# Performance work log

Measured on AMD Instinct MI355X. Metric: run time of the kernel, lower is better.

## Reference

```python
import jax, jax.numpy as jnp
import numpy as np

B, S, D = 2, 2048, 2048
H, KVH, HD = 8, 1, 256          # query heads, kv heads, head_dim (GQA: n_rep = H // KVH)
ROPE_THETA = 10000.0
NEG_INF = -1e9


def setup_inputs() -> dict:
    key = jax.random.key(0)
    k1, k2, k3, k4, k5 = jax.random.split(key, 5)
    hidden_states = jax.random.normal(k1, (B, S, D), dtype=jnp.float32)
    # additive causal mask: 0 where allowed, -inf where masked, shape (B,1,S,S)
    causal = jnp.tril(jnp.ones((S, S), dtype=bool))
    attention_mask = jnp.where(causal, 0.0, NEG_INF).astype(jnp.float32)
    attention_mask = jnp.broadcast_to(attention_mask[None, None], (B, 1, S, S))
    position_ids = jnp.broadcast_to(jnp.arange(S, dtype=jnp.int32)[None, :], (B, S))
    sc = 0.02
    Wq = jax.random.normal(k2, (H * HD, D), dtype=jnp.float32) * sc   # torch Linear weight layout [out,in]
    Wk = jax.random.normal(k3, (KVH * HD, D), dtype=jnp.float32) * sc
    Wv = jax.random.normal(k4, (KVH * HD, D), dtype=jnp.float32) * sc
    Wo = jax.random.normal(k5, (D, H * HD), dtype=jnp.float32) * sc
    return {"hidden_states": hidden_states, "attention_mask": attention_mask,
            "position_ids": position_ids, "Wq": Wq, "Wk": Wk, "Wv": Wv, "Wo": Wo}


def _rotate_half(x):
    x1, x2 = jnp.split(x, 2, axis=-1)
    return jnp.concatenate((-x2, x1), axis=-1)


def _rope_cos_sin(position_ids):
    inv_freq = 1.0 / (ROPE_THETA ** (jnp.arange(0, HD, 2, dtype=jnp.float32) / HD))  # [HD/2]
    freqs = position_ids.astype(jnp.float32)[:, :, None] * inv_freq[None, None, :]   # [B,S,HD/2]
    emb = jnp.concatenate((freqs, freqs), axis=-1)                                   # [B,S,HD]
    return jnp.cos(emb)[:, None], jnp.sin(emb)[:, None]                              # [B,1,S,HD]


def reference(hidden_states, attention_mask, position_ids, Wq, Wk, Wv, Wo):
    q = (hidden_states @ Wq.T).reshape(B, S, H, HD).transpose(0, 2, 1, 3)     # [B,H,S,HD]
    k = (hidden_states @ Wk.T).reshape(B, S, KVH, HD).transpose(0, 2, 1, 3)   # [B,KVH,S,HD]
    v = (hidden_states @ Wv.T).reshape(B, S, KVH, HD).transpose(0, 2, 1, 3)
    cos, sin = _rope_cos_sin(position_ids)
    q = q * cos + _rotate_half(q) * sin
    k = k * cos + _rotate_half(k) * sin
    n_rep = H // KVH
    k = jnp.repeat(k, n_rep, axis=1)                                          # repeat_kv -> [B,H,S,HD]
    v = jnp.repeat(v, n_rep, axis=1)
    scores = jnp.einsum('bhqd,bhkd->bhqk', q, k) / jnp.sqrt(jnp.float32(HD))
    scores = scores + attention_mask
    attn = jax.nn.softmax(scores, axis=-1)                                    # dropout p=0 (eval)
    ctx = jnp.einsum('bhqk,bhkd->bhqd', attn, v)
    ctx = ctx.transpose(0, 2, 1, 3).reshape(B, S, H * HD)
    out = ctx @ Wo.T
    return out, attn
```

## Files before the change

kernel.cpp:

```cpp
#include <hip/hip_runtime.h>
#include <hip/hip_bf16.h>
#include <math.h>

typedef __bf16 bf16_t;
typedef __bf16 bf16x8 __attribute__((ext_vector_type(8)));
typedef float  f32x4  __attribute__((ext_vector_type(4)));

#define DEV __device__ __forceinline__

constexpr int B_   = 2;
constexpr int S_   = 2048;
constexpr int D_   = 2048;
constexpr int H_   = 8;
constexpr int HD_  = 256;
constexpr int NQKV_ = H_ * HD_ + 2 * HD_;
constexpr int TOK_ = B_ * S_;
constexpr int CHK_ = 64 * HD_;

#if defined(__has_builtin)
#if __has_builtin(__builtin_amdgcn_global_load_lds)
#define HAS_GLLDS 1
#endif
#endif

DEV void stage16(const bf16_t* g, bf16_t* l) {
#ifdef HAS_GLLDS
  __builtin_amdgcn_global_load_lds((const __attribute__((address_space(1))) void*)g,
                                   (__attribute__((address_space(3))) void*)l, 16, 0, 0);
#else
  *(bf16x8*)l = *(const bf16x8*)g;
#endif
}

__global__ void cast_inputs(const float* __restrict__ hs, const float* __restrict__ wq,
                            const float* __restrict__ wk, const float* __restrict__ wv,
                            const float* __restrict__ wo,
                            bf16_t* __restrict__ Xb, bf16_t* __restrict__ Wqkvb,
                            bf16_t* __restrict__ Wob) {
  const size_t i = (size_t)blockIdx.x * blockDim.x + threadIdx.x;
  const size_t NHS = (size_t)TOK_ * D_;
  const size_t NWQ = (size_t)H_ * HD_ * D_;
  const size_t NWK = (size_t)HD_ * D_;
  if (i < NHS) Xb[i] = (bf16_t)hs[i];
  if (i < NWQ) { Wqkvb[i] = (bf16_t)wq[i]; Wob[i] = (bf16_t)wo[i]; }
  if (i < NWK) { Wqkvb[NWQ + i] = (bf16_t)wk[i]; Wqkvb[NWQ + NWK + i] = (bf16_t)wv[i]; }
}

template <bool CBF16>
__global__ __launch_bounds__(256, 2)
void gemm_bt(const bf16_t* __restrict__ Ab, const bf16_t* __restrict__ Bg,
             void* __restrict__ Cv, int K, int lda, int ldb, int ldc)
{
  const int bn = blockIdx.x, bm = blockIdx.y;
  const int m0 = bm * 128, n0 = bn * 128;

  __shared__ __align__(16) bf16_t Asm[128 * 32];
  __shared__ __align__(16) bf16_t Bsm[128 * 32];

  const int tid  = threadIdx.x;
  const int l    = tid & 63;
  const int w    = tid >> 6;
  const int wm   = (w >> 1) * 64;
  const int wn   = (w & 1) * 64;
  const int lrow = l & 15;
  const int quad = l >> 4;

  f32x4 acc[4][4] = {};

  for (int k0 = 0; k0 < K; k0 += 32) {
    __syncthreads();
    #pragma unroll
    for (int c = 0; c < 2; ++c) {
      int chunk = c * 256 + tid;
      int row = chunk >> 2, col = (chunk & 3) << 3;
      stage16(Ab + (size_t)(m0 + row) * lda + (k0 + col), &Asm[row * 32 + col]);
      stage16(Bg + (size_t)(n0 + row) * ldb + (k0 + col), &Bsm[row * 32 + col]);
    }
    __syncthreads();

    bf16x8 af[4], bfr[4];
    #pragma unroll
    for (int i = 0; i < 4; ++i)
      af[i] = *(const bf16x8*)&Asm[(wm + i * 16 + lrow) * 32 + quad * 8];
    #pragma unroll
    for (int j = 0; j < 4; ++j)
      bfr[j] = *(const bf16x8*)&Bsm[(wn + j * 16 + lrow) * 32 + quad * 8];
    #pragma unroll
    for (int i = 0; i < 4; ++i)
      #pragma unroll
      for (int j = 0; j < 4; ++j)
        acc[i][j] = __builtin_amdgcn_mfma_f32_16x16x32_bf16(af[i], bfr[j], acc[i][j], 0, 0, 0);
  }

  #pragma unroll
  for (int i = 0; i < 4; ++i) {
    int row = wm + i * 16 + quad * 4;
    #pragma unroll
    for (int j = 0; j < 4; ++j) {
      int col = n0 + wn + j * 16 + lrow;
      #pragma unroll
      for (int r = 0; r < 4; ++r) {
        if (CBF16) ((bf16_t*)Cv)[(size_t)(m0 + row + r) * ldc + col] = (bf16_t)acc[i][j][r];
        else       ((float*) Cv)[(size_t)(m0 + row + r) * ldc + col] = acc[i][j][r];
      }
    }
  }
}

__global__ void rope_kernel(const bf16_t* __restrict__ qkv, const int* __restrict__ pos_ids,
                            bf16_t* __restrict__ Qh, bf16_t* __restrict__ Kb,
                            bf16_t* __restrict__ K2)
{
  const int t = blockIdx.x;
  const int b = t >> 11, s = t & (S_ - 1);
  const int tid = threadIdx.x;
  const int h = tid >> 5, c = tid & 31;
  const float pos = (float)pos_ids[t];
  const int pdbase = (c & 15) * 8;
  float cs[8], sn[8];
  #pragma unroll
  for (int j = 0; j < 8; ++j) {
    float invf = exp2f((float)(pdbase + j) * -0.103810253f);
    float ang = pos * invf;
    cs[j] = cosf(ang); sn[j] = sinf(ang);
  }
  const float sgn = (c < 16) ? -1.0f : 1.0f;
  const bf16_t* base = qkv + (size_t)t * NQKV_;

  {
    bf16x8 x  = *(const bf16x8*)(base + h * HD_ + c * 8);
    bf16x8 xo = *(const bf16x8*)(base + h * HD_ + (c ^ 16) * 8);
    bf16x8 o;
    #pragma unroll
    for (int j = 0; j < 8; ++j)
      o[j] = (bf16_t)((float)x[j] * cs[j] + sgn * (float)xo[j] * sn[j]);
    *(bf16x8*)(Qh + ((size_t)(b * H_ + h) * S_ + s) * HD_ + c * 8) = o;
  }
  if (h == 0) {
    bf16x8 x  = *(const bf16x8*)(base + D_ + c * 8);
    bf16x8 xo = *(const bf16x8*)(base + D_ + (c ^ 16) * 8);
    bf16x8 o;
    #pragma unroll
    for (int j = 0; j < 8; ++j)
      o[j] = (bf16_t)((float)x[j] * cs[j] + sgn * (float)xo[j] * sn[j]);
    *(bf16x8*)(Kb + (size_t)t * HD_ + c * 8) = o;
    const int chunk = s >> 6, key = s & 63;
    *(bf16x8*)(K2 + (size_t)(b * 32 + chunk) * CHK_ + c * 512 + key * 8) = o;
  }
}

__global__ void v_trans(const bf16_t* __restrict__ qkv, bf16_t* __restrict__ V2)
{
  const int blk = blockIdx.x;
  const int s0 = (blk & 31) * 64;
  const int b = blk >> 5;
  const int tid = threadIdx.x;
  __shared__ bf16_t L[64][264];
  #pragma unroll
  for (int it = 0; it < 8; ++it) {
    int gi = it * 256 + tid;
    int r = gi >> 5, cc = gi & 31;
    *(bf16x8*)&L[r][cc * 8] =
        *(const bf16x8*)(qkv + ((size_t)b * S_ + s0 + r) * NQKV_ + (D_ + HD_) + cc * 8);
  }
  __syncthreads();
  bf16_t* out = V2 + (size_t)blk * CHK_;
  #pragma unroll
  for (int it = 0; it < 8; ++it) {
    int G = it * 256 + tid;
    bf16x8 o;
    #pragma unroll
    for (int j = 0; j < 8; ++j) o[j] = L[it * 8 + j][tid];
    *(bf16x8*)(out + (size_t)G * 8) = o;
  }
}

constexpr int PSTR = 136;

DEV void compute_S(const bf16_t* __restrict__ K2g, bf16_t* __restrict__ KV,
                   const bf16x8 aq[8], f32x4 accS[8],
                   int kb, int tid, int lrow, int quad)
{
  #pragma unroll
  for (int half = 0; half < 2; ++half) {
    __syncthreads();
    const bf16_t* src = K2g + (size_t)(kb * 2 + half) * CHK_;
    #pragma unroll
    for (int it = 0; it < 8; ++it) {
      int s = it * 256 + tid;
      stage16(src + (size_t)s * 8, KV + s * 8);
    }
    __syncthreads();
    __builtin_amdgcn_s_setprio(1);
    #pragma unroll
    for (int kk = 0; kk < 8; ++kk) {
      bf16x8 bk[4];
      #pragma unroll
      for (int j = 0; j < 4; ++j)
        bk[j] = *(const bf16x8*)&KV[((kk * 4 + quad) * 64 + j * 16 + lrow) * 8];
      #pragma unroll
      for (int j = 0; j < 4; ++j)
        accS[half * 4 + j] =
            __builtin_amdgcn_mfma_f32_16x16x32_bf16(aq[kk], bk[j], accS[half * 4 + j], 0, 0, 0);
    }
    __builtin_amdgcn_s_setprio(0);
  }
}

__global__ __launch_bounds__(256, 2)
void flash_attn(const bf16_t* __restrict__ Qh, const bf16_t* __restrict__ K2,
                const bf16_t* __restrict__ V2, bf16_t* __restrict__ Ctx,
                float* __restrict__ lsum)
{
  const int idx = blockIdx.x;
  int z, qb;
  if (idx < 256) { z = idx & 15; qb = idx >> 4; }
  else           { int j = idx - 256; z = j & 15; qb = 31 - (j >> 4); }
  const int b = z >> 3, h = z & 7;
  const int q0 = qb * 64;
  const bf16_t* Qg  = Qh + ((size_t)z * S_ + q0) * HD_;
  const bf16_t* K2g = K2 + (size_t)b * 32 * CHK_;
  const bf16_t* V2g = V2 + (size_t)b * 32 * CHK_;

  __shared__ __align__(16) bf16_t KV[64 * 256];
  __shared__ __align__(16) bf16_t Pst[4 * 16 * PSTR];

  const int tid = threadIdx.x;
  const int w = tid >> 6, l = tid & 63;
  const int lrow = l & 15, quad = l >> 4;
  const int nkb = (qb >> 1) + 1;
  const float scale = 0.0625f;

  bf16x8 aq[8];
  const bf16_t* qrow = Qg + (size_t)(w * 16 + lrow) * HD_ + quad * 8;
  #pragma unroll
  for (int kk = 0; kk < 8; ++kk) aq[kk] = *(const bf16x8*)(qrow + kk * 32);

  const int rowg0 = q0 + w * 16 + quad * 4;
  float lp[4] = {0.f, 0.f, 0.f, 0.f};
  f32x4 accO[16] = {};
  bf16_t* pw = &Pst[w * 16 * PSTR];

  for (int kb = 0; kb < nkb; ++kb) {
    f32x4 accS[8] = {};
    compute_S(K2g, KV, aq, accS, kb, tid, lrow, quad);

    #pragma unroll
    for (int r = 0; r < 4; ++r) {
      #pragma unroll
      for (int j = 0; j < 8; ++j) {
        int col = kb * 128 + j * 16 + lrow;
        float p = (col <= rowg0 + r) ? __expf(accS[j][r] * scale) : 0.f;
        lp[r] += p;
        pw[(quad * 4 + r) * PSTR + j * 16 + lrow] = (bf16_t)p;
      }
    }
    bf16x8 ap[4];
    #pragma unroll
    for (int kk2 = 0; kk2 < 4; ++kk2)
      ap[kk2] = *(const bf16x8*)&pw[lrow * PSTR + kk2 * 32 + quad * 8];

    #pragma unroll
    for (int half = 0; half < 2; ++half) {
      __syncthreads();
      const bf16_t* src = V2g + (size_t)(kb * 2 + half) * CHK_;
      #pragma unroll
      for (int it = 0; it < 8; ++it) {
        int s = it * 256 + tid;
        stage16(src + (size_t)s * 8, KV + s * 8);
      }
      __syncthreads();
      __builtin_amdgcn_s_setprio(1);
      #pragma unroll
      for (int kkl = 0; kkl < 2; ++kkl) {
        #pragma unroll
        for (int j2 = 0; j2 < 16; ++j2) {
          bf16x8 bv = *(const bf16x8*)&KV[((kkl * 4 + quad) * 256 + j2 * 16 + lrow) * 8];
          accO[j2] = __builtin_amdgcn_mfma_f32_16x16x32_bf16(ap[half * 2 + kkl], bv, accO[j2], 0, 0, 0);
        }
      }
      __builtin_amdgcn_s_setprio(0);
    }
  }

  #pragma unroll
  for (int r = 0; r < 4; ++r) {
    #pragma unroll
    for (int o = 1; o < 16; o <<= 1) lp[r] += __shfl_xor(lp[r], o, 64);
  }
  float inv[4];
  #pragma unroll
  for (int r = 0; r < 4; ++r) inv[r] = 1.0f / lp[r];

  #pragma unroll
  for (int j2 = 0; j2 < 16; ++j2) {
    #pragma unroll
    for (int r = 0; r < 4; ++r) {
      int rowq = q0 + w * 16 + quad * 4 + r;
      Ctx[((size_t)b * S_ + rowq) * D_ + h * HD_ + j2 * 16 + lrow] = (bf16_t)(accO[j2][r] * inv[r]);
    }
  }
  if (lrow == 0) {
    #pragma unroll
    for (int r = 0; r < 4; ++r) lsum[(size_t)z * S_ + rowg0 + r] = lp[r];
  }
}

__global__ __launch_bounds__(256, 2)
void p_writer(const bf16_t* __restrict__ Qh, const bf16_t* __restrict__ Kbp,
              const float* __restrict__ lsum, float* __restrict__ attn)
{
  const int bn = blockIdx.x, bm = blockIdx.y, z = blockIdx.z;
  const int m0 = bm * 128, n0 = bn * 128;
  float* Pg = attn + (size_t)z * S_ * S_;
  const int tid = threadIdx.x;

  if (bn > bm) {
    #pragma unroll
    for (int it = 0; it < 16; ++it) {
      int idx = it * 256 + tid;
      int row = idx >> 5, c4 = idx & 31;
      *(f32x4*)&Pg[(size_t)(m0 + row) * S_ + n0 + c4 * 4] = f32x4{0.f, 0.f, 0.f, 0.f};
    }
    return;
  }

  const bf16_t* Ab = Qh + (size_t)z * S_ * HD_;
  const bf16_t* Bg = Kbp + (size_t)(z >> 3) * S_ * HD_;

  __shared__ __align__(16) bf16_t Asm[128 * 32];
  __shared__ __align__(16) bf16_t Bsm[128 * 32];

  const int l    = tid & 63;
  const int w    = tid >> 6;
  const int wm   = (w >> 1) * 64;
  const int wn   = (w & 1) * 64;
  const int lrow = l & 15;
  const int quad = l >> 4;

  f32x4 acc[4][4] = {};

  for (int k0 = 0; k0 < HD_; k0 += 32) {
    __syncthreads();
    #pragma unroll
    for (int c = 0; c < 2; ++c) {
      int chunk = c * 256 + tid;
      int row = chunk >> 2, col = (chunk & 3) << 3;
      stage16(Ab + (size_t)(m0 + row) * HD_ + (k0 + col), &Asm[row * 32 + col]);
      stage16(Bg + (size_t)(n0 + row) * HD_ + (k0 + col), &Bsm[row * 32 + col]);
    }
    __syncthreads();

    bf16x8 af[4], bfr[4];
    #pragma unroll
    for (int i = 0; i < 4; ++i)
      af[i] = *(const bf16x8*)&Asm[(wm + i * 16 + lrow) * 32 + quad * 8];
    #pragma unroll
    for (int j = 0; j < 4; ++j)
      bfr[j] = *(const bf16x8*)&Bsm[(wn + j * 16 + lrow) * 32 + quad * 8];
    #pragma unroll
    for (int i = 0; i < 4; ++i)
      #pragma unroll
      for (int j = 0; j < 4; ++j)
        acc[i][j] = __builtin_amdgcn_mfma_f32_16x16x32_bf16(af[i], bfr[j], acc[i][j], 0, 0, 0);
  }

  const float scale = 0.0625f;
  #pragma unroll
  for (int i = 0; i < 4; ++i) {
    int row = m0 + wm + i * 16 + quad * 4;
    #pragma unroll
    for (int r = 0; r < 4; ++r) {
      const float il = 1.0f / lsum[(size_t)z * S_ + row + r];
      float* prow = &Pg[(size_t)(row + r) * S_];
      #pragma unroll
      for (int j = 0; j < 4; ++j) {
        int col = n0 + wn + j * 16 + lrow;
        prow[col] = (col <= row + r) ? __expf(acc[i][j][r] * scale) * il : 0.f;
      }
    }
  }
}

extern "C" void kernel_launch(void* const* d_in, const int* in_sizes, int n_in,
                              void* d_out, int out_size, void* d_ws, size_t ws_size,
                              hipStream_t stream)
{
  const float* hs  = (const float*)d_in[0];
  const int*   pos = (const int*)d_in[2];
  const float* wq  = (const float*)d_in[3];
  const float* wk  = (const float*)d_in[4];
  const float* wv  = (const float*)d_in[5];
  const float* wo  = (const float*)d_in[6];

  float* out  = (float*)d_out;
  float* attn = out + (size_t)TOK_ * D_;

  char* ws = (char*)d_ws;
  bf16_t* Xb    = (bf16_t*)(ws);
  bf16_t* Wqkvb = (bf16_t*)(ws + 16777216);
  bf16_t* Wob   = (bf16_t*)(ws + 27262976);
  bf16_t* QKVb  = (bf16_t*)(ws + 35651584);
  bf16_t* Qh    = (bf16_t*)(ws + 56623104);
  bf16_t* Kb    = (bf16_t*)(ws + 73400320);
  bf16_t* V2    = (bf16_t*)(ws + 75497472);
  bf16_t* Ctx   = (bf16_t*)(ws + 77594624);
  float*  lsum  = (float* )(ws + 94371840);
  bf16_t* K2    = (bf16_t*)(ws + 94502912);

  cast_inputs<<<(TOK_ * D_) / 256, 256, 0, stream>>>(hs, wq, wk, wv, wo, Xb, Wqkvb, Wob);
  gemm_bt<true><<<dim3(NQKV_ / 128, TOK_ / 128), 256, 0, stream>>>(
      Xb, Wqkvb, QKVb, D_, D_, D_, NQKV_);
  rope_kernel<<<TOK_, 256, 0, stream>>>(QKVb, pos, Qh, Kb, K2);
  v_trans<<<B_ * 32, 256, 0, stream>>>(QKVb, V2);
  flash_attn<<<512, 256, 0, stream>>>(Qh, K2, V2, Ctx, lsum);
  p_writer<<<dim3(S_ / 128, S_ / 128, B_ * H_), 256, 0, stream>>>(Qh, Kb, lsum, attn);
  gemm_bt<false><<<dim3(D_ / 128, TOK_ / 128), 256, 0, stream>>>(
      Ctx, Wob, out, D_, D_, D_, D_);
}
```

Measured before the change: 622.1 us.

## Use K=64 swizzled LDS tiles, XCD-aware block remap, and overlap V staging with softmax

Moves the shared GEMM mainloop into a helper that stages 64-wide K tiles with an XOR swizzle, halving barrier count and targeting LDS bank conflicts. The gemm and p_writer grids are remapped so consecutive logical tiles land on the same XCD, aiming for better L2 reuse. The attention kernel now issues the first V chunk load before the exp/P-store phase so the global load overlaps softmax work. LDS use per block doubles, which may reduce occupancy, and the remap in p_writer hardcodes the grid size.

```diff
diff --git a/kernel.cpp b/kernel.cpp
--- a/kernel.cpp
+++ b/kernel.cpp
@@ -46,16 +46,55 @@
   if (i < NWK) { Wqkvb[NWQ + i] = (bf16_t)wk[i]; Wqkvb[NWQ + NWK + i] = (bf16_t)wv[i]; }
 }
 
+DEV void tile_k64(const bf16_t* __restrict__ Ab, const bf16_t* __restrict__ Bg,
+                  int K, int lda, int ldb, int m0, int n0,
+                  bf16_t* Asm, bf16_t* Bsm, f32x4 acc[4][4],
+                  int tid, int lrow, int quad, int wm, int wn)
+{
+  const int sw = (lrow & 1) << 2;
+  for (int k0 = 0; k0 < K; k0 += 64) {
+    __syncthreads();
+    #pragma unroll
+    for (int c = 0; c < 4; ++c) {
+      int chunk = c * 256 + tid;
+      int row = chunk >> 3, pg = chunk & 7;
+      int g = pg ^ ((row & 1) << 2);
+      stage16(Ab + (size_t)(m0 + row) * lda + (k0 + g * 8), &Asm[chunk * 8]);
+      stage16(Bg + (size_t)(n0 + row) * ldb + (k0 + g * 8), &Bsm[chunk * 8]);
+    }
+    __syncthreads();
+    #pragma unroll
+    for (int kk = 0; kk < 2; ++kk) {
+      bf16x8 af[4], bfr[4];
+      #pragma unroll
+      for (int i = 0; i < 4; ++i)
+        af[i] = *(const bf16x8*)&Asm[(wm + i * 16 + lrow) * 64 + ((quad + kk * 4) ^ sw) * 8];
+      #pragma unroll
+      for (int j = 0; j < 4; ++j)
+        bfr[j] = *(const bf16x8*)&Bsm[(wn + j * 16 + lrow) * 64 + ((quad + kk * 4) ^ sw) * 8];
+      #pragma unroll
+      for (int i = 0; i < 4; ++i)
+        #pragma unroll
+        for (int j = 0; j < 4; ++j)
+          acc[i][j] = __builtin_amdgcn_mfma_f32_16x16x32_bf16(af[i], bfr[j], acc[i][j], 0, 0, 0);
+    }
+  }
+}
+
 template <bool CBF16>
 __global__ __launch_bounds__(256, 2)
 void gemm_bt(const bf16_t* __restrict__ Ab, const bf16_t* __restrict__ Bg,
              void* __restrict__ Cv, int K, int lda, int ldb, int ldc)
 {
-  const int bn = blockIdx.x, bm = blockIdx.y;
+  const int nwg = gridDim.x * gridDim.y;
+  const int w0  = blockIdx.y * gridDim.x + blockIdx.x;
+  const int q   = nwg >> 3;
+  const int logical = (w0 & 7) * q + (w0 >> 3);
+  const int bm = logical / gridDim.x, bn = logical % gridDim.x;
   const int m0 = bm * 128, n0 = bn * 128;
 
-  __shared__ __align__(16) bf16_t Asm[128 * 32];
-  __shared__ __align__(16) bf16_t Bsm[128 * 32];
+  __shared__ __align__(16) bf16_t Asm[128 * 64];
+  __shared__ __align__(16) bf16_t Bsm[128 * 64];
 
   const int tid  = threadIdx.x;
   const int l    = tid & 63;
@@ -66,31 +105,7 @@
   const int quad = l >> 4;
 
   f32x4 acc[4][4] = {};
-
-  for (int k0 = 0; k0 < K; k0 += 32) {
-    __syncthreads();
-    #pragma unroll
-    for (int c = 0; c < 2; ++c) {
-      int chunk = c * 256 + tid;
-      int row = chunk >> 2, col = (chunk & 3) << 3;
-      stage16(Ab + (size_t)(m0 + row) * lda + (k0 + col), &Asm[row * 32 + col]);
-      stage16(Bg + (size_t)(n0 + row) * ldb + (k0 + col), &Bsm[row * 32 + col]);
-    }
-    __syncthreads();
-
-    bf16x8 af[4], bfr[4];
-    #pragma unroll
-    for (int i = 0; i < 4; ++i)
-      af[i] = *(const bf16x8*)&Asm[(wm + i * 16 + lrow) * 32 + quad * 8];
-    #pragma unroll
-    for (int j = 0; j < 4; ++j)
-      bfr[j] = *(const bf16x8*)&Bsm[(wn + j * 16 + lrow) * 32 + quad * 8];
-    #pragma unroll
-    for (int i = 0; i < 4; ++i)
-      #pragma unroll
-      for (int j = 0; j < 4; ++j)
-        acc[i][j] = __builtin_amdgcn_mfma_f32_16x16x32_bf16(af[i], bfr[j], acc[i][j], 0, 0, 0);
-  }
+  tile_k64(Ab, Bg, K, lda, ldb, m0, n0, Asm, Bsm, acc, tid, lrow, quad, wm, wn);
 
   #pragma unroll
   for (int i = 0; i < 4; ++i) {
@@ -244,6 +259,16 @@
   for (int kb = 0; kb < nkb; ++kb) {
     f32x4 accS[8] = {};
     compute_S(K2g, KV, aq, accS, kb, tid, lrow, quad);
+    __syncthreads();
+
+    {
+      const bf16_t* src = V2g + (size_t)(kb * 2 + 0) * CHK_;
+      #pragma unroll
+      for (int it = 0; it < 8; ++it) {
+        int s = it * 256 + tid;
+        stage16(src + (size_t)s * 8, KV + s * 8);
+      }
+    }
 
     #pragma unroll
     for (int r = 0; r < 4; ++r) {
@@ -260,27 +285,38 @@
     for (int kk2 = 0; kk2 < 4; ++kk2)
       ap[kk2] = *(const bf16x8*)&pw[lrow * PSTR + kk2 * 32 + quad * 8];
 
-    #pragma unroll
-    for (int half = 0; half < 2; ++half) {
-      __syncthreads();
-      const bf16_t* src = V2g + (size_t)(kb * 2 + half) * CHK_;
+    __syncthreads();
+    __builtin_amdgcn_s_setprio(1);
+    #pragma unroll
+    for (int kkl = 0; kkl < 2; ++kkl) {
+      #pragma unroll
+      for (int j2 = 0; j2 < 16; ++j2) {
+        bf16x8 bv = *(const bf16x8*)&KV[((kkl * 4 + quad) * 256 + j2 * 16 + lrow) * 8];
+        accO[j2] = __builtin_amdgcn_mfma_f32_16x16x32_bf16(ap[kkl], bv, accO[j2], 0, 0, 0);
+      }
+    }
+    __builtin_amdgcn_s_setprio(0);
+
+    __syncthreads();
+    {
+      const bf16_t* src = V2g + (size_t)(kb * 2 + 1) * CHK_;
       #pragma unroll
       for (int it = 0; it < 8; ++it) {
         int s = it * 256 + tid;
         stage16(src + (size_t)s * 8, KV + s * 8);
       }
-      __syncthreads();
-      __builtin_amdgcn_s_setprio(1);
-      #pragma unroll
-      for (int kkl = 0; kkl < 2; ++kkl) {
-        #pragma unroll
-        for (int j2 = 0; j2 < 16; ++j2) {
-          bf16x8 bv = *(const bf16x8*)&KV[((kkl * 4 + quad) * 256 + j2 * 16 + lrow) * 8];
-          accO[j2] = __builtin_amdgcn_mfma_f32_16x16x32_bf16(ap[half * 2 + kkl], bv, accO[j2], 0, 0, 0);
-        }
-      }
-      __builtin_amdgcn_s_setprio(0);
-    }
+    }
+    __syncthreads();
+    __builtin_amdgcn_s_setprio(1);
+    #pragma unroll
+    for (int kkl = 0; kkl < 2; ++kkl) {
+      #pragma unroll
+      for (int j2 = 0; j2 < 16; ++j2) {
+        bf16x8 bv = *(const bf16x8*)&KV[((kkl * 4 + quad) * 256 + j2 * 16 + lrow) * 8];
+        accO[j2] = __builtin_amdgcn_mfma_f32_16x16x32_bf16(ap[2 + kkl], bv, accO[j2], 0, 0, 0);
+      }
+    }
+    __builtin_amdgcn_s_setprio(0);
   }
 
   #pragma unroll
@@ -310,7 +346,9 @@
 void p_writer(const bf16_t* __restrict__ Qh, const bf16_t* __restrict__ Kbp,
               const float* __restrict__ lsum, float* __restrict__ attn)
 {
-  const int bn = blockIdx.x, bm = blockIdx.y, z = blockIdx.z;
+  const int w0 = (blockIdx.z * gridDim.y + blockIdx.y) * gridDim.x + blockIdx.x;
+  const int logical = (w0 & 7) * 512 + (w0 >> 3);
+  const int z = logical >> 8, bm = (logical >> 4) & 15, bn = logical & 15;
   const int m0 = bm * 128, n0 = bn * 128;
   float* Pg = attn + (size_t)z * S_ * S_;
   const int tid = threadIdx.x;
@@ -328,8 +366,8 @@
   const bf16_t* Ab = Qh + (size_t)z * S_ * HD_;
   const bf16_t* Bg = Kbp + (size_t)(z >> 3) * S_ * HD_;
 
-  __shared__ __align__(16) bf16_t Asm[128 * 32];
-  __shared__ __align__(16) bf16_t Bsm[128 * 32];
+  __shared__ __align__(16) bf16_t Asm[128 * 64];
+  __shared__ __align__(16) bf16_t Bsm[128 * 64];
 
   const int l    = tid & 63;
   const int w    = tid >> 6;
@@ -339,31 +377,7 @@
   const int quad = l >> 4;
 
   f32x4 acc[4][4] = {};
-
-  for (int k0 = 0; k0 < HD_; k0 += 32) {
-    __syncthreads();
-    #pragma unroll
-    for (int c = 0; c < 2; ++c) {
-      int chunk = c * 256 + tid;
-      int row = chunk >> 2, col = (chunk & 3) << 3;
-      stage16(Ab + (size_t)(m0 + row) * HD_ + (k0 + col), &Asm[row * 32 + col]);
-      stage16(Bg + (size_t)(n0 + row) * HD_ + (k0 + col), &Bsm[row * 32 + col]);
-    }
-    __syncthreads();
-
-    bf16x8 af[4], bfr[4];
-    #pragma unroll
-    for (int i = 0; i < 4; ++i)
-      af[i] = *(const bf16x8*)&Asm[(wm + i * 16 + lrow) * 32 + quad * 8];
-    #pragma unroll
-    for (int j = 0; j < 4; ++j)
-      bfr[j] = *(const bf16x8*)&Bsm[(wn + j * 16 + lrow) * 32 + quad * 8];
-    #pragma unroll
-    for (int i = 0; i < 4; ++i)
-      #pragma unroll
-      for (int j = 0; j < 4; ++j)
-        acc[i][j] = __builtin_amdgcn_mfma_f32_16x16x32_bf16(af[i], bfr[j], acc[i][j], 0, 0, 0);
-  }
+  tile_k64(Ab, Bg, HD_, HD_, HD_, m0, n0, Asm, Bsm, acc, tid, lrow, quad, wm, wn);
 
   const float scale = 0.0625f;
   #pragma unroll
```

Measured after the change: 591.0 us. 5.0% less time.
